# Optimization experiments

Measured on AMD Instinct MI355X. Metric: run time of the kernel, lower is better.

Reference implementation:

```python
import jax, jax.numpy as jnp
import numpy as np

EMBED, HEADS, WIN, UP = 180, 6, 16, 4
HDIM = EMBED // HEADS

def _win_part(x, ws):
    # x: [B, H, W, C] -> [B*(H//ws)*(W//ws), ws, ws, C]
    B, H, W, C = x.shape
    x = x.reshape(B, H // ws, ws, W // ws, ws, C).transpose(0, 1, 3, 2, 4, 5)
    return x.reshape(-1, ws, ws, C)

def _win_rev(w, ws, H, W):
    # inverse of _win_part
    C = w.shape[-1]
    B = w.shape[0] // ((H // ws) * (W // ws))
    x = w.reshape(B, H // ws, W // ws, ws, ws, C).transpose(0, 1, 3, 2, 4, 5)
    return x.reshape(B, H, W, C)

def _ln(x, g, b):
    mu = x.mean(-1, keepdims=True)
    v = ((x - mu) ** 2).mean(-1, keepdims=True)
    return (x - mu) * jax.lax.rsqrt(v + 1e-5) * g + b

def _forward(gumbel_u, x, sel1_w, sel1_b, sel2_w, sel2_b, sel3_w, sel3_b,
             embed_w, embed_b, ln1_g, ln1_b, qkv_w, qkv_b, proj_w, proj_b,
             ln2_g, ln2_b, mlp1_w, mlp1_b, mlp2_w, mlp2_b, up_w, up_b):
    B, C, H, W = x.shape
    ws = H // 4                                     # 64 -> 16 tiles per image
    tiles = _win_part(x.transpose(0, 2, 3, 1), ws)  # [T, ws, ws, C]
    T = tiles.shape[0]
    # --- TileSelection (pooled MLP router) ---
    pooled = tiles.reshape(T, 8, ws // 8, 8, ws // 8, C).mean((2, 4)).reshape(T, 8 * 8 * C)
    f1 = pooled @ sel1_w + sel1_b
    f2 = jax.nn.relu(f1) @ sel2_w + sel2_b
    f3 = jax.nn.relu(f2) @ sel3_w + sel3_b          # [T, 2] routing logits
    # --- hard gumbel-softmax with straight-through estimator (tau=1) ---
    g = -jnp.log(-jnp.log(gumbel_u + 1e-10) + 1e-10)
    y_soft = jax.nn.softmax(f3 + g, axis=-1)
    y_hard = jax.nn.one_hot(jnp.argmax(y_soft, -1), 2, dtype=y_soft.dtype)
    pi = jax.lax.stop_gradient(y_hard - y_soft) + y_soft
    mask = pi[:, 1]                                 # 1 -> transformer expert
    # --- TR expert (SwinIR-style block, dense dispatch over all tiles) ---
    tok = tiles.reshape(T, ws * ws, C) @ embed_w + embed_b   # [T, 4096, 180]
    h = _ln(tok, ln1_g, ln1_b)
    hw = _win_part(h.reshape(T, ws, ws, EMBED), WIN).reshape(-1, WIN * WIN, EMBED)
    Nw, L = hw.shape[0], WIN * WIN
    qkv = (hw @ qkv_w + qkv_b).reshape(Nw, L, 3, HEADS, HDIM)
    q, k, v = qkv[:, :, 0], qkv[:, :, 1], qkv[:, :, 2]
    attn = jax.nn.softmax(jnp.einsum('nlhd,nmhd->nhlm', q, k) / np.sqrt(HDIM).astype(np.float32), axis=-1)
    av = jnp.einsum('nhlm,nmhd->nlhd', attn, v).reshape(Nw, L, EMBED)
    av = av @ proj_w + proj_b
    av = _win_rev(av.reshape(Nw, WIN, WIN, EMBED), WIN, ws, ws).reshape(T, ws * ws, EMBED)
    tok = tok + av
    h2 = _ln(tok, ln2_g, ln2_b)
    tok = tok + jax.nn.gelu(h2 @ mlp1_w + mlp1_b) @ mlp2_w + mlp2_b
    # pixelshuffle x4 upsample: 180 -> 3*4*4
    up = (tok @ up_w + up_b).reshape(T, ws, ws, UP, UP, C)
    up = up.transpose(0, 1, 3, 2, 4, 5).reshape(T, ws * UP, ws * UP, C)
    # --- cheap expert: bicubic x4 ---
    neg = jax.image.resize(tiles, (T, ws * UP, ws * UP, C), method='bicubic')
    # --- combine per-tile and reassemble ---
    m = mask[:, None, None, None]
    sr_tiles = m * up + (1.0 - m) * neg             # [T, 4ws, 4ws, C]
    sr = _win_rev(sr_tiles, H, H * UP, W * UP)      # [B, 4H, 4W, C]
    return sr.transpose(0, 3, 1, 2), f3, f2, f1

def setup_inputs() -> dict:
    key = jax.random.key(0)
    ks = jax.random.split(key, 16)
    B, C, H, W = 1, 3, 256, 256
    T = B * 16
    p = lambda k, s: jax.random.normal(k, s, jnp.float32) * 0.02
    return {
        'x': jax.random.normal(ks[0], (B, C, H, W), jnp.float32),
        'gumbel_u': jax.random.uniform(ks[1], (T, 2), jnp.float32),
        'sel1_w': p(ks[2], (192, 64)), 'sel1_b': jnp.zeros((64,), jnp.float32),
        'sel2_w': p(ks[3], (64, 32)), 'sel2_b': jnp.zeros((32,), jnp.float32),
        'sel3_w': p(ks[4], (32, 2)), 'sel3_b': jnp.zeros((2,), jnp.float32),
        'embed_w': p(ks[5], (3, EMBED)), 'embed_b': jnp.zeros((EMBED,), jnp.float32),
        'ln1_g': jnp.ones((EMBED,), jnp.float32), 'ln1_b': jnp.zeros((EMBED,), jnp.float32),
        'qkv_w': p(ks[6], (EMBED, 3 * EMBED)), 'qkv_b': jnp.zeros((3 * EMBED,), jnp.float32),
        'proj_w': p(ks[7], (EMBED, EMBED)), 'proj_b': jnp.zeros((EMBED,), jnp.float32),
        'ln2_g': jnp.ones((EMBED,), jnp.float32), 'ln2_b': jnp.zeros((EMBED,), jnp.float32),
        'mlp1_w': p(ks[8], (EMBED, 2 * EMBED)), 'mlp1_b': jnp.zeros((2 * EMBED,), jnp.float32),
        'mlp2_w': p(ks[9], (2 * EMBED, EMBED)), 'mlp2_b': jnp.zeros((EMBED,), jnp.float32),
        'up_w': p(ks[10], (EMBED, 3 * UP * UP)), 'up_b': jnp.zeros((3 * UP * UP,), jnp.float32),
    }

def reference(x, gumbel_u, sel1_w, sel1_b, sel2_w, sel2_b, sel3_w, sel3_b,
              embed_w, embed_b, ln1_g, ln1_b, qkv_w, qkv_b, proj_w, proj_b,
              ln2_g, ln2_b, mlp1_w, mlp1_b, mlp2_w, mlp2_b, up_w, up_b):
    return _forward(gumbel_u, x, sel1_w, sel1_b, sel2_w, sel2_b, sel3_w, sel3_b,
                    embed_w, embed_b, ln1_g, ln1_b, qkv_w, qkv_b, proj_w, proj_b,
                    ln2_g, ln2_b, mlp1_w, mlp1_b, mlp2_w, mlp2_b, up_w, up_b)
```

## Files before the change

kernel.cpp:

```cpp
#include <hip/hip_runtime.h>
#include <hip/hip_bf16.h>
#include <cstdint>

typedef __hip_bfloat16 bf16;
typedef __attribute__((ext_vector_type(8))) short short8;
typedef __attribute__((ext_vector_type(4))) short short4v;
typedef __attribute__((ext_vector_type(4))) float f32x4;
typedef __attribute__((ext_vector_type(2))) unsigned int uint2v;

__device__ __forceinline__ float bf2f(bf16 v) { return __bfloat162float(v); }
__device__ __forceinline__ bf16  f2bf(float v) { return __float2bfloat16(v); }
__device__ __forceinline__ float rbf(short s) {
  union { uint32_t u; float f; } c; c.u = ((uint32_t)(uint16_t)s) << 16; return c.f;
}
__device__ __forceinline__ uint32_t pack2(float a, float b) {
  bf16 x = f2bf(a), y = f2bf(b);
  return (uint32_t)(*(uint16_t*)&x) | ((uint32_t)(*(uint16_t*)&y) << 16);
}
__device__ __forceinline__ uint2v pack4(float a, float b, float c, float d) {
  uint2v r; r[0] = pack2(a, b); r[1] = pack2(c, d); return r;
}
__device__ __forceinline__ int swz(int row, int g) { return g ^ (row & 7); }

__device__ __forceinline__ int win_to_token(int m) {
  int n = m >> 8, l = m & 255;
  int t = n >> 4, win = n & 15;
  int wi = win >> 2, wj = win & 3;
  int u = l >> 4, v = l & 15;
  return (t << 12) | ((wi * 16 + u) << 6) | (wj * 16 + v);
}

__global__ __launch_bounds__(256) void k_packsel(
    const float* __restrict__ qkvw, const float* __restrict__ projw,
    const float* __restrict__ mlp1w, const float* __restrict__ mlp2w,
    const float* __restrict__ upw, const float* __restrict__ qkvb,
    bf16* __restrict__ Bt_qkv, bf16* __restrict__ Bt_proj,
    bf16* __restrict__ Bt_mlp1, bf16* __restrict__ Bt_mlp2,
    bf16* __restrict__ Bt_up, float* __restrict__ biasq,
    const float* __restrict__ x, const float* __restrict__ gu,
    const float* __restrict__ s1w, const float* __restrict__ s1b,
    const float* __restrict__ s2w, const float* __restrict__ s2b,
    const float* __restrict__ s3w, const float* __restrict__ s3b,
    float* __restrict__ f1o, float* __restrict__ f2o, float* __restrict__ f3o,
    float* __restrict__ maskp) {
  if (blockIdx.x < 1203) {
    int idx = blockIdx.x * 256 + threadIdx.x;
    const int e0 = 576 * 192, e1 = e0 + 192 * 192, e2 = e1 + 384 * 192,
              e3 = e2 + 192 * 384, e4 = e3 + 64 * 192, e5 = e4 + 576;
    if (idx < e0) {
      int np = idx / 192, k = idx % 192;
      int buf = np / 192, colp = np % 192;
      int hd = colp >> 5, dd = colp & 31;
      float v = 0.f;
      if (dd < 30 && k < 180) v = qkvw[(size_t)k * 540 + buf * 180 + hd * 30 + dd];
      Bt_qkv[idx] = f2bf(v);
    } else if (idx < e1) {
      int off = idx - e0; int n = off / 192, kp = off % 192;
      int hd = kp >> 5, dd = kp & 31;
      float v = (dd < 30 && n < 180) ? projw[(size_t)(hd * 30 + dd) * 180 + n] : 0.f;
      Bt_proj[off] = f2bf(v);
    } else if (idx < e2) {
      int off = idx - e1; int n = off / 192, k = off % 192;
      Bt_mlp1[off] = f2bf((k < 180 && n < 360) ? mlp1w[(size_t)k * 360 + n] : 0.f);
    } else if (idx < e3) {
      int off = idx - e2; int n = off / 384, k = off % 384;
      Bt_mlp2[off] = f2bf((k < 360 && n < 180) ? mlp2w[(size_t)k * 180 + n] : 0.f);
    } else if (idx < e4) {
      int off = idx - e3; int n = off / 192, k = off % 192;
      Bt_up[off] = f2bf((k < 180 && n < 48) ? upw[(size_t)k * 48 + n] : 0.f);
    } else if (idx < e5) {
      int np = idx - e4;
      int buf = np / 192, colp = np % 192;
      int hd = colp >> 5, dd = colp & 31;
      biasq[np] = (dd < 30) ? qkvb[buf * 180 + hd * 30 + dd] : 0.f;
    }
    return;
  }
  int t = blockIdx.x - 1203;
  int tid = threadIdx.x;
  int th = t >> 2, tw = t & 3;
  __shared__ float pooled[192];
  __shared__ float red[256];
  __shared__ float f1s[64], f2s[32], f3s[2];
  if (tid < 192) {
    int ch = tid % 3, j = (tid / 3) & 7, i = tid / 24;
    const float* xp = x + ch * 65536 + (th * 64 + i * 8) * 256 + (tw * 64 + j * 8);
    float s = 0.f;
#pragma unroll
    for (int a = 0; a < 8; ++a)
#pragma unroll
      for (int b = 0; b < 8; ++b) s += xp[a * 256 + b];
    pooled[tid] = s * (1.0f / 64.0f);
  }
  __syncthreads();
  {
    int o = tid & 63, part = tid >> 6;
    float s = 0.f;
    for (int k = part * 48; k < part * 48 + 48; ++k) s = fmaf(pooled[k], s1w[k * 64 + o], s);
    red[tid] = s;
  }
  __syncthreads();
  if (tid < 64) {
    float v = red[tid] + red[tid + 64] + red[tid + 128] + red[tid + 192] + s1b[tid];
    f1o[t * 64 + tid] = v;
    f1s[tid] = fmaxf(v, 0.f);
  }
  __syncthreads();
  {
    int o = tid & 31, part = tid >> 5;
    float s = 0.f;
    for (int k = part * 8; k < part * 8 + 8; ++k) s = fmaf(f1s[k], s2w[k * 32 + o], s);
    red[tid] = s;
  }
  __syncthreads();
  if (tid < 32) {
    float v = s2b[tid];
#pragma unroll
    for (int p = 0; p < 8; ++p) v += red[tid + p * 32];
    f2o[t * 32 + tid] = v;
    f2s[tid] = fmaxf(v, 0.f);
  }
  __syncthreads();
  if (tid < 2) {
    float s = s3b[tid];
    for (int k = 0; k < 32; ++k) s = fmaf(f2s[k], s3w[k * 2 + tid], s);
    f3o[t * 2 + tid] = s;
    f3s[tid] = s;
  }
  __syncthreads();
  if (tid == 0) {
    float g0 = -logf(-logf(gu[t * 2 + 0] + 1e-10f) + 1e-10f);
    float g1 = -logf(-logf(gu[t * 2 + 1] + 1e-10f) + 1e-10f);
    maskp[t] = (f3s[1] + g1 > f3s[0] + g0) ? 1.0f : 0.0f;
  }
}

__global__ __launch_bounds__(256) void k_embed(
    const float* __restrict__ x, const float* __restrict__ ew,
    const float* __restrict__ eb, const float* __restrict__ g1,
    const float* __restrict__ b1, bf16* __restrict__ tok,
    bf16* __restrict__ Aq) {
  int wrow = blockIdx.x * 4 + (threadIdx.x >> 6);
  int lane = threadIdx.x & 63;
  int token = win_to_token(wrow);
  int t = token >> 12, p = token & 4095;
  int r = p >> 6, c = p & 63;
  int gh = (t >> 2) * 64 + r, gw = (t & 3) * 64 + c;
  float x0 = x[gh * 256 + gw];
  float x1 = x[65536 + gh * 256 + gw];
  float x2 = x[131072 + gh * 256 + gw];
  float v[3];
  float s = 0.f, s2 = 0.f;
#pragma unroll
  for (int i = 0; i < 3; ++i) {
    int e = lane + i * 64;
    float vv = 0.f;
    if (e < 180) {
      vv = eb[e];
      vv = fmaf(x0, ew[e], vv);
      vv = fmaf(x1, ew[180 + e], vv);
      vv = fmaf(x2, ew[360 + e], vv);
      tok[(size_t)wrow * 180 + e] = f2bf(vv);
      s += vv; s2 = fmaf(vv, vv, s2);
    }
    v[i] = vv;
  }
#pragma unroll
  for (int off = 32; off; off >>= 1) { s += __shfl_xor(s, off); s2 += __shfl_xor(s2, off); }
  float mu = s * (1.f / 180.f);
  float rs = rsqrtf(s2 * (1.f / 180.f) - mu * mu + 1e-5f);
#pragma unroll
  for (int i = 0; i < 3; ++i) {
    int e = lane + i * 64;
    if (e < 192) {
      float a = (e < 180) ? ((v[i] - mu) * rs * g1[e] + b1[e]) : 0.f;
      Aq[(size_t)wrow * 192 + e] = f2bf(a);
    }
  }
}

__global__ __launch_bounds__(256) void k_qkv2(
    const bf16* __restrict__ A, const bf16* __restrict__ Bt,
    const float* __restrict__ biasq, bf16* __restrict__ Qp,
    bf16* __restrict__ Kp, bf16* __restrict__ Vp) {
  __shared__ bf16 Bs[2][64 * 192];
  const int tid = threadIdx.x;
  const int w = tid >> 6, l = tid & 63;
  const int lr = l & 15, lk = l >> 4;
  const int rbase = blockIdx.x * 128 + w * 32 + lr;

  short8 fa[2][6];
#pragma unroll
  for (int i = 0; i < 2; ++i) {
    const bf16* Ab = A + (size_t)(rbase + i * 16) * 192 + lk * 8;
#pragma unroll
    for (int ks = 0; ks < 6; ++ks) fa[i][ks] = *(const short8*)(Ab + ks * 32);
  }

  {
    const bf16* src = Bt;
#pragma unroll
    for (int it = 0; it < 6; ++it) {
      int c = tid + it * 256;
      int n = c / 24, g = c % 24;
      *(short8*)&Bs[0][n * 192 + swz(n, g) * 8] = *(const short8*)(src + n * 192 + g * 8);
    }
  }

  for (int nt = 0; nt < 9; ++nt) {
    __syncthreads();
    if (nt < 8) {
      const bf16* src = Bt + (size_t)(nt + 1) * 64 * 192;
      bf16* dstb = Bs[(nt + 1) & 1];
#pragma unroll
      for (int it = 0; it < 6; ++it) {
        int c = tid + it * 256;
        int n = c / 24, g = c % 24;
        *(short8*)&dstb[n * 192 + swz(n, g) * 8] = *(const short8*)(src + n * 192 + g * 8);
      }
    }
    const bf16* Bb = Bs[nt & 1];
    f32x4 acc[2][4];
#pragma unroll
    for (int i = 0; i < 2; ++i)
#pragma unroll
      for (int j = 0; j < 4; ++j) acc[i][j] = (f32x4){0.f, 0.f, 0.f, 0.f};
#pragma unroll
    for (int ks = 0; ks < 6; ++ks) {
      short8 fb[4];
#pragma unroll
      for (int j = 0; j < 4; ++j) {
        int rn = j * 16 + lr;
        fb[j] = *(const short8*)&Bb[rn * 192 + swz(rn, ks * 4 + lk) * 8];
      }
#pragma unroll
      for (int i = 0; i < 2; ++i)
#pragma unroll
        for (int j = 0; j < 4; ++j)
          acc[i][j] = __builtin_amdgcn_mfma_f32_16x16x32_bf16(fb[j], fa[i][ks], acc[i][j], 0, 0, 0);
    }
    bf16* dst = (nt < 3) ? Qp : (nt < 6) ? Kp : Vp;
    int c0 = (nt % 3) * 64;
#pragma unroll
    for (int i = 0; i < 2; ++i) {
      int row = rbase + i * 16;
#pragma unroll
      for (int j = 0; j < 4; ++j) {
        int np = nt * 64 + j * 16 + lk * 4;
        f32x4 bv = *(const f32x4*)&biasq[np];
        *(uint2v*)(dst + (size_t)row * 192 + c0 + j * 16 + lk * 4) =
            pack4(acc[i][j][0] + bv[0], acc[i][j][1] + bv[1],
                  acc[i][j][2] + bv[2], acc[i][j][3] + bv[3]);
      }
    }
  }
}

__global__ __launch_bounds__(256) void k_attn2(
    const bf16* __restrict__ Qp, const bf16* __restrict__ Kp,
    const bf16* __restrict__ Vp, bf16* __restrict__ av) {
  const int blk = blockIdx.x;
  const int win = blk / 6, hd = blk % 6;
  const int tid = threadIdx.x;
  const int w = tid >> 6, l = tid & 63;
  const int lr = l & 15, lk = l >> 4;
  const float scale = 0.18257418583505536f;

  __shared__ bf16 Ks[256][40];
  __shared__ bf16 Vs[32][264];
  __shared__ bf16 Ps[4][16][264];

  {
    const bf16* src = Kp + (size_t)(win * 256 + tid) * 192 + hd * 32;
#pragma unroll
    for (int c = 0; c < 4; ++c)
      *(short8*)&Ks[tid][c * 8] = *(const short8*)(src + c * 8);
  }
  {
    const bf16* src = Vp + (size_t)(win * 256 + tid) * 192 + hd * 32;
    short8 vv[4];
#pragma unroll
    for (int c = 0; c < 4; ++c) vv[c] = *(const short8*)(src + c * 8);
#pragma unroll
    for (int c = 0; c < 4; ++c)
#pragma unroll
      for (int e = 0; e < 8; ++e)
        *(short*)&Vs[c * 8 + e][tid] = vv[c][e];
  }
  __syncthreads();

  for (int qt = 0; qt < 4; ++qt) {
    const int qbase = qt * 64 + w * 16;
    short8 fq = *(const short8*)(Qp + (size_t)(win * 256 + qbase + lr) * 192 + hd * 32 + lk * 8);
    f32x4 accS[16];
#pragma unroll
    for (int kt = 0; kt < 16; ++kt) {
      short8 fk = *(const short8*)(&Ks[kt * 16 + lr][lk * 8]);
      accS[kt] = __builtin_amdgcn_mfma_f32_16x16x32_bf16(
          fk, fq, (f32x4){0.f, 0.f, 0.f, 0.f}, 0, 0, 0);
    }
    float mraw = -1e30f;
#pragma unroll
    for (int kt = 0; kt < 16; ++kt)
#pragma unroll
      for (int r = 0; r < 4; ++r) mraw = fmaxf(mraw, accS[kt][r]);
    mraw = fmaxf(mraw, __shfl_xor(mraw, 16));
    mraw = fmaxf(mraw, __shfl_xor(mraw, 32));
    const float mc = mraw * scale;
    float lsum = 0.f;
#pragma unroll
    for (int kt = 0; kt < 16; ++kt) {
      float p0 = __expf(fmaf(accS[kt][0], scale, -mc));
      float p1 = __expf(fmaf(accS[kt][1], scale, -mc));
      float p2 = __expf(fmaf(accS[kt][2], scale, -mc));
      float p3 = __expf(fmaf(accS[kt][3], scale, -mc));
      lsum += (p0 + p1) + (p2 + p3);
      *(uint32_t*)&Ps[w][lr][kt * 16 + lk * 4]     = pack2(p0, p1);
      *(uint32_t*)&Ps[w][lr][kt * 16 + lk * 4 + 2] = pack2(p2, p3);
    }
    lsum += __shfl_xor(lsum, 16);
    lsum += __shfl_xor(lsum, 32);
    __syncthreads();
    f32x4 accO0 = (f32x4){0.f, 0.f, 0.f, 0.f};
    f32x4 accO1 = (f32x4){0.f, 0.f, 0.f, 0.f};
#pragma unroll
    for (int ks = 0; ks < 8; ++ks) {
      short8 fp  = *(const short8*)(&Ps[w][lr][ks * 32 + lk * 8]);
      short8 fv0 = *(const short8*)(&Vs[lr][ks * 32 + lk * 8]);
      short8 fv1 = *(const short8*)(&Vs[16 + lr][ks * 32 + lk * 8]);
      accO0 = __builtin_amdgcn_mfma_f32_16x16x32_bf16(fv0, fp, accO0, 0, 0, 0);
      accO1 = __builtin_amdgcn_mfma_f32_16x16x32_bf16(fv1, fp, accO1, 0, 0, 0);
    }
    float invl = 1.f / lsum;
    bf16* avrow = av + (size_t)(win * 256 + qbase + lr) * 192 + hd * 32;
    *(uint2v*)(avrow + lk * 4) =
        pack4(accO0[0] * invl, accO0[1] * invl, accO0[2] * invl, accO0[3] * invl);
    *(uint2v*)(avrow + 16 + lk * 4) =
        pack4(accO1[0] * invl, accO1[1] * invl, accO1[2] * invl, accO1[3] * invl);
    __syncthreads();
  }
}

__global__ __launch_bounds__(256) void k_post(
    const bf16* __restrict__ av, const bf16* __restrict__ tok,
    const bf16* __restrict__ Btp, const float* __restrict__ pb,
    const float* __restrict__ g2, const float* __restrict__ b2,
    const bf16* __restrict__ Bt1, const float* __restrict__ b1m,
    const bf16* __restrict__ Bt2, const float* __restrict__ b2m,
    const bf16* __restrict__ Btu, const float* __restrict__ bu,
    bf16* __restrict__ up) {
  __shared__ bf16 Bs[64 * 192];
  __shared__ bf16 T2[64 * 192];
  __shared__ bf16 Hm[64 * 192];
  const int tid = threadIdx.x;
  const int w = tid >> 6, l = tid & 63;
  const int lr = l & 15, lk = l >> 4;
  const int row_l = w * 16 + lr;
  const int row_g = blockIdx.x * 64 + row_l;
  const int half = (lk & 1) * 4;

  short8 fa[6];
  {
    const bf16* ab = av + (size_t)row_g * 192 + lk * 8;
#pragma unroll
    for (int ks = 0; ks < 6; ++ks) fa[ks] = *(const short8*)(ab + ks * 32);
  }

  f32x4 t2v[3][4];
#pragma unroll
  for (int nt = 0; nt < 3; ++nt) {
    __syncthreads();
    for (int c = tid; c < 1536; c += 256) {
      int n = c / 24, g = c % 24;
      *(short8*)&Bs[n * 192 + swz(n, g) * 8] =
          *(const short8*)(Btp + (size_t)(nt * 64 + n) * 192 + g * 8);
    }
    __syncthreads();
    f32x4 acc[4];
#pragma unroll
    for (int j = 0; j < 4; ++j) acc[j] = (f32x4){0.f, 0.f, 0.f, 0.f};
#pragma unroll
    for (int ks = 0; ks < 6; ++ks) {
      short8 fb[4];
#pragma unroll
      for (int j = 0; j < 4; ++j) {
        int rn = j * 16 + lr;
        fb[j] = *(const short8*)&Bs[rn * 192 + swz(rn, ks * 4 + lk) * 8];
      }
#pragma unroll
      for (int j = 0; j < 4; ++j)
        acc[j] = __builtin_amdgcn_mfma_f32_16x16x32_bf16(fb[j], fa[ks], acc[j], 0, 0, 0);
    }
#pragma unroll
    for (int j = 0; j < 4; ++j) {
      int n = nt * 64 + j * 16 + lk * 4;
      if (n < 180) {
        f32x4 bv = *(const f32x4*)&pb[n];
        short4v tv = *(const short4v*)(tok + (size_t)row_g * 180 + n);
#pragma unroll
        for (int q = 0; q < 4; ++q) t2v[nt][j][q] = acc[j][q] + bv[q] + rbf(tv[q]);
      } else {
        t2v[nt][j] = (f32x4){0.f, 0.f, 0.f, 0.f};
      }
    }
  }

  {
    float s = 0.f, s2 = 0.f;
#pragma unroll
    for (int nt = 0; nt < 3; ++nt)
#pragma unroll
      for (int j = 0; j < 4; ++j)
#pragma unroll
        for (int q = 0; q < 4; ++q) { float v = t2v[nt][j][q]; s += v; s2 = fmaf(v, v, s2); }
    s += __shfl_xor(s, 16);  s += __shfl_xor(s, 32);
    s2 += __shfl_xor(s2, 16); s2 += __shfl_xor(s2, 32);
    float mu = s * (1.f / 180.f);
    float rs = rsqrtf(s2 * (1.f / 180.f) - mu * mu + 1e-5f);
#pragma unroll
    for (int nt = 0; nt < 3; ++nt)
#pragma unroll
      for (int j = 0; j < 4; ++j) {
        int n = nt * 64 + j * 16 + lk * 4;
        float h[4] = {0.f, 0.f, 0.f, 0.f};
        if (n < 180) {
          f32x4 gv = *(const f32x4*)&g2[n];
          f32x4 bv = *(const f32x4*)&b2[n];
#pragma unroll
          for (int q = 0; q < 4; ++q) h[q] = (t2v[nt][j][q] - mu) * rs * gv[q] + bv[q];
        }
        int g = nt * 8 + j * 2 + (lk >> 1);
        *(uint2v*)&Hm[row_l * 192 + swz(row_l, g) * 8 + half] = pack4(h[0], h[1], h[2], h[3]);
      }
  }
  __syncthreads();
  short8 fh[6];
#pragma unroll
  for (int ks = 0; ks < 6; ++ks)
    fh[ks] = *(const short8*)&Hm[row_l * 192 + swz(row_l, ks * 4 + lk) * 8];

  f32x4 acc2[3][4];
#pragma unroll
  for (int t = 0; t < 3; ++t)
#pragma unroll
    for (int j = 0; j < 4; ++j) acc2[t][j] = (f32x4){0.f, 0.f, 0.f, 0.f};
#pragma unroll
  for (int nt = 0; nt < 6; ++nt) {
    __syncthreads();
    for (int c = tid; c < 1536; c += 256) {
      int n = c / 24, g = c % 24;
      *(short8*)&Bs[n * 192 + swz(n, g) * 8] =
          *(const short8*)(Bt1 + (size_t)(nt * 64 + n) * 192 + g * 8);
    }
    __syncthreads();
    f32x4 acc1[4];
#pragma unroll
    for (int j = 0; j < 4; ++j) acc1[j] = (f32x4){0.f, 0.f, 0.f, 0.f};
#pragma unroll
    for (int ks = 0; ks < 6; ++ks) {
      short8 fb[4];
#pragma unroll
      for (int j = 0; j < 4; ++j) {
        int rn = j * 16 + lr;
        fb[j] = *(const short8*)&Bs[rn * 192 + swz(rn, ks * 4 + lk) * 8];
      }
#pragma unroll
      for (int j = 0; j < 4; ++j)
        acc1[j] = __builtin_amdgcn_mfma_f32_16x16x32_bf16(fb[j], fh[ks], acc1[j], 0, 0, 0);
    }
#pragma unroll
    for (int j = 0; j < 4; ++j) {
      int n = nt * 64 + j * 16 + lk * 4;
      float m4[4] = {0.f, 0.f, 0.f, 0.f};
      if (n < 360) {
        f32x4 bv = *(const f32x4*)&b1m[n];
#pragma unroll
        for (int q = 0; q < 4; ++q) {
          float v = acc1[j][q] + bv[q];
          float u = 0.7978845608028654f * (v + 0.044715f * v * v * v);
          m4[q] = v / (1.f + __expf(-2.f * u));
        }
      }
      int g = j * 2 + (lk >> 1);
      *(uint2v*)&Hm[row_l * 192 + swz(row_l, g) * 8 + half] = pack4(m4[0], m4[1], m4[2], m4[3]);
    }
    __syncthreads();
    for (int c = tid; c < 1536; c += 256) {
      int n = c / 8, g = c % 8;
      *(short8*)&Bs[n * 64 + swz(n, g) * 8] =
          *(const short8*)(Bt2 + (size_t)n * 384 + nt * 64 + g * 8);
    }
    __syncthreads();
    short8 fm[2];
#pragma unroll
    for (int s = 0; s < 2; ++s)
      fm[s] = *(const short8*)&Hm[row_l * 192 + swz(row_l, s * 4 + lk) * 8];
#pragma unroll
    for (int s = 0; s < 2; ++s)
#pragma unroll
      for (int t = 0; t < 3; ++t)
#pragma unroll
        for (int j = 0; j < 4; ++j) {
          int rn = t * 64 + j * 16 + lr;
          short8 fb2 = *(const short8*)&Bs[rn * 64 + swz(rn, s * 4 + lk) * 8];
          acc2[t][j] = __builtin_amdgcn_mfma_f32_16x16x32_bf16(fb2, fm[s], acc2[t][j], 0, 0, 0);
        }
  }

#pragma unroll
  for (int t = 0; t < 3; ++t)
#pragma unroll
    for (int j = 0; j < 4; ++j) {
      int n = t * 64 + j * 16 + lk * 4;
      float o4[4] = {0.f, 0.f, 0.f, 0.f};
      if (n < 180) {
        f32x4 bv = *(const f32x4*)&b2m[n];
#pragma unroll
        for (int q = 0; q < 4; ++q) o4[q] = acc2[t][j][q] + bv[q] + t2v[t][j][q];
      }
      int g = t * 8 + j * 2 + (lk >> 1);
      *(uint2v*)&T2[row_l * 192 + swz(row_l, g) * 8 + half] = pack4(o4[0], o4[1], o4[2], o4[3]);
    }
  __syncthreads();

  for (int c = tid; c < 1536; c += 256) {
    int n = c / 24, g = c % 24;
    *(short8*)&Bs[n * 192 + swz(n, g) * 8] =
        *(const short8*)(Btu + (size_t)n * 192 + g * 8);
  }
  __syncthreads();
  short8 ft[6];
#pragma unroll
  for (int ks = 0; ks < 6; ++ks)
    ft[ks] = *(const short8*)&T2[row_l * 192 + swz(row_l, ks * 4 + lk) * 8];
  f32x4 acc3[3];
#pragma unroll
  for (int j = 0; j < 3; ++j) acc3[j] = (f32x4){0.f, 0.f, 0.f, 0.f};
#pragma unroll
  for (int ks = 0; ks < 6; ++ks) {
    short8 fb[3];
#pragma unroll
    for (int j = 0; j < 3; ++j) {
      int rn = j * 16 + lr;
      fb[j] = *(const short8*)&Bs[rn * 192 + swz(rn, ks * 4 + lk) * 8];
    }
#pragma unroll
    for (int j = 0; j < 3; ++j)
      acc3[j] = __builtin_amdgcn_mfma_f32_16x16x32_bf16(fb[j], ft[ks], acc3[j], 0, 0, 0);
  }
#pragma unroll
  for (int j = 0; j < 3; ++j) {
    int n = j * 16 + lk * 4;
    f32x4 bv = *(const f32x4*)&bu[n];
    *(uint2v*)(up + (size_t)row_g * 48 + n) =
        pack4(acc3[j][0] + bv[0], acc3[j][1] + bv[1], acc3[j][2] + bv[2], acc3[j][3] + bv[3]);
  }
}

__device__ const float c_cubw[4][4] = {
    {-0.0439453125f, 0.3896484375f, 0.7275390625f, -0.0732421875f},
    {-0.0068359375f, 0.0908203125f, 0.9638671875f, -0.0478515625f},
    {-0.0478515625f, 0.9638671875f, 0.0908203125f, -0.0068359375f},
    {-0.0732421875f, 0.7275390625f, 0.3896484375f, -0.0439453125f},
};

__device__ __forceinline__ void cubw(int r, int ph, float* w, int& base) {
  base = r + ((ph < 2) ? -2 : -1);
  float sum = 0.f;
#pragma unroll
  for (int i = 0; i < 4; ++i) {
    int idx = base + i;
    float wi = (idx >= 0 && idx < 64) ? c_cubw[ph][i] : 0.f;
    w[i] = wi; sum += wi;
  }
  float inv = 1.f / sum;
#pragma unroll
  for (int i = 0; i < 4; ++i) w[i] *= inv;
}

__global__ __launch_bounds__(256) void k_blend(
    const bf16* __restrict__ up, const float* __restrict__ x,
    const float* __restrict__ maskp, float* __restrict__ sr) {
  int idx = blockIdx.x * 256 + threadIdx.x;
  int ch = idx >> 20;
  int rem = idx & 1048575;
  int gR = rem >> 10, gC = rem & 1023;
  int th = gR >> 8, tw = gC >> 8;
  int t = th * 4 + tw;
  int R = gR & 255, C = gC & 255;
  int r = R >> 2, a = R & 3, c = C >> 2, b = C & 3;
  float m = maskp[t];
  float outv;
  if (m > 0.5f) {
    int wi = r >> 4, u = r & 15, wj = c >> 4, v = c & 15;
    int wrow = (t * 16 + wi * 4 + wj) * 256 + u * 16 + v;
    outv = bf2f(up[(size_t)wrow * 48 + a * 12 + b * 3 + ch]);
  } else {
    float wy[4], wx[4];
    int yb, xb;
    cubw(r, a, wy, yb);
    cubw(c, b, wx, xb);
    const float* xc = x + ch * 65536;
    float neg = 0.f;
#pragma unroll
    for (int i = 0; i < 4; ++i) {
      int yi = yb + i;
      if (yi < 0 || yi > 63) continue;
      float rowsum = 0.f;
#pragma unroll
      for (int j = 0; j < 4; ++j) {
        int xj = xb + j;
        if (xj < 0 || xj > 63) continue;
        rowsum = fmaf(wx[j], xc[(th * 64 + yi) * 256 + tw * 64 + xj], rowsum);
      }
      neg = fmaf(wy[i], rowsum, neg);
    }
    outv = neg;
  }
  sr[idx] = outv;
}

extern "C" void kernel_launch(void* const* d_in, const int* in_sizes, int n_in,
                              void* d_out, int out_size, void* d_ws, size_t ws_size,
                              hipStream_t stream) {
  const float* x     = (const float*)d_in[0];
  const float* gu    = (const float*)d_in[1];
  const float* s1w   = (const float*)d_in[2];
  const float* s1b   = (const float*)d_in[3];
  const float* s2w   = (const float*)d_in[4];
  const float* s2b   = (const float*)d_in[5];
  const float* s3w   = (const float*)d_in[6];
  const float* s3b   = (const float*)d_in[7];
  const float* ew    = (const float*)d_in[8];
  const float* ebias = (const float*)d_in[9];
  const float* ln1g  = (const float*)d_in[10];
  const float* ln1b  = (const float*)d_in[11];
  const float* qkvw  = (const float*)d_in[12];
  const float* qkvb  = (const float*)d_in[13];
  const float* projw = (const float*)d_in[14];
  const float* projb = (const float*)d_in[15];
  const float* ln2g  = (const float*)d_in[16];
  const float* ln2b  = (const float*)d_in[17];
  const float* mlp1w = (const float*)d_in[18];
  const float* mlp1b = (const float*)d_in[19];
  const float* mlp2w = (const float*)d_in[20];
  const float* mlp2b = (const float*)d_in[21];
  const float* upw   = (const float*)d_in[22];
  const float* upb   = (const float*)d_in[23];

  float* out = (float*)d_out;
  float* sr  = out;
  float* f3o = out + 3145728;
  float* f2o = f3o + 32;
  float* f1o = f2o + 512;

  char* ws = (char*)d_ws;
  bf16* tok  = (bf16*)(ws);
  bf16* ABuf = (bf16*)(ws + 23592960);
  bf16* Qp   = (bf16*)(ws + 48758784);
  bf16* Kp   = (bf16*)(ws + 73924608);
  bf16* Vp   = (bf16*)(ws + 99090432);
  float* maskp   = (float*)(ws + 124256256);
  bf16* Bt_qkv  = (bf16*)(ws + 124256320);
  bf16* Bt_proj = (bf16*)(ws + 124477504);
  bf16* Bt_mlp1 = (bf16*)(ws + 124551232);
  bf16* Bt_mlp2 = (bf16*)(ws + 124698688);
  bf16* Bt_up   = (bf16*)(ws + 124846144);
  float* biasq  = (float*)(ws + 124870720);
  bf16* up      = (bf16*)(ws + 124873088);
  bf16* av = ABuf;

  k_packsel<<<1219, 256, 0, stream>>>(qkvw, projw, mlp1w, mlp2w, upw, qkvb,
                                      Bt_qkv, Bt_proj, Bt_mlp1, Bt_mlp2, Bt_up, biasq,
                                      x, gu, s1w, s1b, s2w, s2b, s3w, s3b,
                                      f1o, f2o, f3o, maskp);
  k_embed<<<16384, 256, 0, stream>>>(x, ew, ebias, ln1g, ln1b, tok, ABuf);
  k_qkv2<<<512, 256, 0, stream>>>(ABuf, Bt_qkv, biasq, Qp, Kp, Vp);
  k_attn2<<<1536, 256, 0, stream>>>(Qp, Kp, Vp, av);
  k_post<<<1024, 256, 0, stream>>>(av, tok, Bt_proj, projb, ln2g, ln2b,
                                   Bt_mlp1, mlp1b, Bt_mlp2, mlp2b, Bt_up, upb, up);
  k_blend<<<12288, 256, 0, stream>>>(up, x, maskp, sr);
}
```

Measured before the change: 226.8 us.

## Shuffle softmax probabilities in registers and alias LDS buffers in post kernel

The attention kernel no longer stages the probability matrix through shared memory. It rebuilds the MFMA operand layout with cross-lane shuffles, which also removes two block-wide barriers per query tile. The post kernel reuses the Hm buffer in place of a separate T2 buffer and adds one barrier before the reuse. Both changes cut LDS footprint, which can allow more resident blocks, at the cost of many extra shuffle instructions and higher register pressure from the 32 packed values held per lane.

```diff
diff --git a/kernel.cpp b/kernel.cpp
--- a/kernel.cpp
+++ b/kernel.cpp
@@ -7,6 +7,7 @@
 typedef __attribute__((ext_vector_type(4))) short short4v;
 typedef __attribute__((ext_vector_type(4))) float f32x4;
 typedef __attribute__((ext_vector_type(2))) unsigned int uint2v;
+typedef __attribute__((ext_vector_type(4))) unsigned int uint4v;
 
 __device__ __forceinline__ float bf2f(bf16 v) { return __bfloat162float(v); }
 __device__ __forceinline__ bf16  f2bf(float v) { return __float2bfloat16(v); }
@@ -256,7 +257,7 @@
   }
 }
 
-__global__ __launch_bounds__(256) void k_attn2(
+__global__ __launch_bounds__(256) void k_attn3(
     const bf16* __restrict__ Qp, const bf16* __restrict__ Kp,
     const bf16* __restrict__ Vp, bf16* __restrict__ av) {
   const int blk = blockIdx.x;
@@ -268,7 +269,6 @@
 
   __shared__ bf16 Ks[256][40];
   __shared__ bf16 Vs[32][264];
-  __shared__ bf16 Ps[4][16][264];
 
   {
     const bf16* src = Kp + (size_t)(win * 256 + tid) * 192 + hd * 32;
@@ -288,6 +288,10 @@
         *(short*)&Vs[c * 8 + e][tid] = vv[c][e];
   }
   __syncthreads();
+
+  const int a0lane = lr + 32 * (lk & 1);
+  const int a1lane = a0lane + 16;
+  const bool hi = (lk >= 2);
 
   for (int qt = 0; qt < 4; ++qt) {
     const int qbase = qt * 64 + w * 16;
@@ -308,6 +312,7 @@
     mraw = fmaxf(mraw, __shfl_xor(mraw, 32));
     const float mc = mraw * scale;
     float lsum = 0.f;
+    uint32_t u0[16], u1[16];
 #pragma unroll
     for (int kt = 0; kt < 16; ++kt) {
       float p0 = __expf(fmaf(accS[kt][0], scale, -mc));
@@ -315,17 +320,30 @@
       float p2 = __expf(fmaf(accS[kt][2], scale, -mc));
       float p3 = __expf(fmaf(accS[kt][3], scale, -mc));
       lsum += (p0 + p1) + (p2 + p3);
-      *(uint32_t*)&Ps[w][lr][kt * 16 + lk * 4]     = pack2(p0, p1);
-      *(uint32_t*)&Ps[w][lr][kt * 16 + lk * 4 + 2] = pack2(p2, p3);
+      u0[kt] = pack2(p0, p1);
+      u1[kt] = pack2(p2, p3);
     }
     lsum += __shfl_xor(lsum, 16);
     lsum += __shfl_xor(lsum, 32);
-    __syncthreads();
     f32x4 accO0 = (f32x4){0.f, 0.f, 0.f, 0.f};
     f32x4 accO1 = (f32x4){0.f, 0.f, 0.f, 0.f};
 #pragma unroll
     for (int ks = 0; ks < 8; ++ks) {
-      short8 fp  = *(const short8*)(&Ps[w][lr][ks * 32 + lk * 8]);
+      uint32_t A0 = (uint32_t)__shfl((int)u0[2 * ks], a0lane);
+      uint32_t A1 = (uint32_t)__shfl((int)u1[2 * ks], a0lane);
+      uint32_t A2 = (uint32_t)__shfl((int)u0[2 * ks], a1lane);
+      uint32_t A3 = (uint32_t)__shfl((int)u1[2 * ks], a1lane);
+      uint32_t B0 = (uint32_t)__shfl((int)u0[2 * ks + 1], a0lane);
+      uint32_t B1 = (uint32_t)__shfl((int)u1[2 * ks + 1], a0lane);
+      uint32_t B2 = (uint32_t)__shfl((int)u0[2 * ks + 1], a1lane);
+      uint32_t B3 = (uint32_t)__shfl((int)u1[2 * ks + 1], a1lane);
+      uint4v Dv;
+      Dv[0] = hi ? B0 : A0;
+      Dv[1] = hi ? B1 : A1;
+      Dv[2] = hi ? B2 : A2;
+      Dv[3] = hi ? B3 : A3;
+      short8 fp;
+      __builtin_memcpy(&fp, &Dv, 16);
       short8 fv0 = *(const short8*)(&Vs[lr][ks * 32 + lk * 8]);
       short8 fv1 = *(const short8*)(&Vs[16 + lr][ks * 32 + lk * 8]);
       accO0 = __builtin_amdgcn_mfma_f32_16x16x32_bf16(fv0, fp, accO0, 0, 0, 0);
@@ -337,7 +355,6 @@
         pack4(accO0[0] * invl, accO0[1] * invl, accO0[2] * invl, accO0[3] * invl);
     *(uint2v*)(avrow + 16 + lk * 4) =
         pack4(accO1[0] * invl, accO1[1] * invl, accO1[2] * invl, accO1[3] * invl);
-    __syncthreads();
   }
 }
 
@@ -350,7 +367,6 @@
     const bf16* __restrict__ Btu, const float* __restrict__ bu,
     bf16* __restrict__ up) {
   __shared__ bf16 Bs[64 * 192];
-  __shared__ bf16 T2[64 * 192];
   __shared__ bf16 Hm[64 * 192];
   const int tid = threadIdx.x;
   const int w = tid >> 6, l = tid & 63;
@@ -507,6 +523,7 @@
         }
   }
 
+  __syncthreads();
 #pragma unroll
   for (int t = 0; t < 3; ++t)
 #pragma unroll
@@ -519,7 +536,7 @@
         for (int q = 0; q < 4; ++q) o4[q] = acc2[t][j][q] + bv[q] + t2v[t][j][q];
       }
       int g = t * 8 + j * 2 + (lk >> 1);
-      *(uint2v*)&T2[row_l * 192 + swz(row_l, g) * 8 + half] = pack4(o4[0], o4[1], o4[2], o4[3]);
+      *(uint2v*)&Hm[row_l * 192 + swz(row_l, g) * 8 + half] = pack4(o4[0], o4[1], o4[2], o4[3]);
     }
   __syncthreads();
 
@@ -532,7 +549,7 @@
   short8 ft[6];
 #pragma unroll
   for (int ks = 0; ks < 6; ++ks)
-    ft[ks] = *(const short8*)&T2[row_l * 192 + swz(row_l, ks * 4 + lk) * 8];
+    ft[ks] = *(const short8*)&Hm[row_l * 192 + swz(row_l, ks * 4 + lk) * 8];
   f32x4 acc3[3];
 #pragma unroll
   for (int j = 0; j < 3; ++j) acc3[j] = (f32x4){0.f, 0.f, 0.f, 0.f};
@@ -676,7 +693,7 @@
                                       f1o, f2o, f3o, maskp);
   k_embed<<<16384, 256, 0, stream>>>(x, ew, ebias, ln1g, ln1b, tok, ABuf);
   k_qkv2<<<512, 256, 0, stream>>>(ABuf, Bt_qkv, biasq, Qp, Kp, Vp);
-  k_attn2<<<1536, 256, 0, stream>>>(Qp, Kp, Vp, av);
+  k_attn3<<<1536, 256, 0, stream>>>(Qp, Kp, Vp, av);
   k_post<<<1024, 256, 0, stream>>>(av, tok, Bt_proj, projb, ln2g, ln2b,
                                    Bt_mlp1, mlp1b, Bt_mlp2, mlp2b, Bt_up, upb, up);
   k_blend<<<12288, 256, 0, stream>>>(up, x, maskp, sr);
```

Result: slower. 245.6 us (+8.3%).

## Double-buffer weight staging in k_post to overlap loads with MFMA

Applied to the files above, without the earlier changes.

Splits the shared weight buffer in k_post into two halves, so the next weight tile (proj, mlp1, mlp2 slice, upsample) is copied into one half while MFMAs read the other. This removes one barrier per step and lets global loads overlap compute. The separate T2 buffer is dropped and Hm is reused, which keeps shared memory the same. The cost is a more intricate barrier ordering, which risks races if any buffer is reused too early.

```diff
diff --git a/kernel.cpp b/kernel.cpp
--- a/kernel.cpp
+++ b/kernel.cpp
@@ -349,8 +349,7 @@
     const bf16* __restrict__ Bt2, const float* __restrict__ b2m,
     const bf16* __restrict__ Btu, const float* __restrict__ bu,
     bf16* __restrict__ up) {
-  __shared__ bf16 Bs[64 * 192];
-  __shared__ bf16 T2[64 * 192];
+  __shared__ bf16 Bs[2][64 * 192];
   __shared__ bf16 Hm[64 * 192];
   const int tid = threadIdx.x;
   const int w = tid >> 6, l = tid & 63;
@@ -359,6 +358,30 @@
   const int row_g = blockIdx.x * 64 + row_l;
   const int half = (lk & 1) * 4;
 
+#define STAGE_A(srcp, dstb)                                               \
+  {                                                                       \
+    const bf16* _s = (srcp);                                              \
+    bf16* _d = (dstb);                                                    \
+    _Pragma("unroll")                                                     \
+    for (int it = 0; it < 6; ++it) {                                      \
+      int c = tid + it * 256;                                             \
+      int n = c / 24, g = c % 24;                                         \
+      *(short8*)&_d[n * 192 + swz(n, g) * 8] =                            \
+          *(const short8*)(_s + (size_t)n * 192 + g * 8);                 \
+    }                                                                     \
+  }
+#define STAGE_S(ntv, dstb)                                                \
+  {                                                                       \
+    bf16* _d = (dstb);                                                    \
+    _Pragma("unroll")                                                     \
+    for (int it = 0; it < 6; ++it) {                                      \
+      int c = tid + it * 256;                                             \
+      int n = c / 8, g = c % 8;                                           \
+      *(short8*)&_d[n * 64 + swz(n, g) * 8] =                             \
+          *(const short8*)(Bt2 + (size_t)n * 384 + (ntv) * 64 + g * 8);   \
+    }                                                                     \
+  }
+
   short8 fa[6];
   {
     const bf16* ab = av + (size_t)row_g * 192 + lk * 8;
@@ -367,15 +390,15 @@
   }
 
   f32x4 t2v[3][4];
+
+  STAGE_A(Btp, Bs[0]);
+
 #pragma unroll
   for (int nt = 0; nt < 3; ++nt) {
     __syncthreads();
-    for (int c = tid; c < 1536; c += 256) {
-      int n = c / 24, g = c % 24;
-      *(short8*)&Bs[n * 192 + swz(n, g) * 8] =
-          *(const short8*)(Btp + (size_t)(nt * 64 + n) * 192 + g * 8);
-    }
-    __syncthreads();
+    if (nt < 2) { STAGE_A(Btp + (size_t)(nt + 1) * 64 * 192, Bs[(nt + 1) & 1]); }
+    else        { STAGE_A(Bt1, Bs[1]); }
+    const bf16* Bb = Bs[nt & 1];
     f32x4 acc[4];
 #pragma unroll
     for (int j = 0; j < 4; ++j) acc[j] = (f32x4){0.f, 0.f, 0.f, 0.f};
@@ -385,7 +408,7 @@
 #pragma unroll
       for (int j = 0; j < 4; ++j) {
         int rn = j * 16 + lr;
-        fb[j] = *(const short8*)&Bs[rn * 192 + swz(rn, ks * 4 + lk) * 8];
+        fb[j] = *(const short8*)&Bb[rn * 192 + swz(rn, ks * 4 + lk) * 8];
       }
 #pragma unroll
       for (int j = 0; j < 4; ++j)
@@ -433,80 +456,79 @@
         *(uint2v*)&Hm[row_l * 192 + swz(row_l, g) * 8 + half] = pack4(h[0], h[1], h[2], h[3]);
       }
   }
-  __syncthreads();
+
   short8 fh[6];
-#pragma unroll
-  for (int ks = 0; ks < 6; ++ks)
-    fh[ks] = *(const short8*)&Hm[row_l * 192 + swz(row_l, ks * 4 + lk) * 8];
-
   f32x4 acc2[3][4];
 #pragma unroll
   for (int t = 0; t < 3; ++t)
 #pragma unroll
     for (int j = 0; j < 4; ++j) acc2[t][j] = (f32x4){0.f, 0.f, 0.f, 0.f};
+
 #pragma unroll
   for (int nt = 0; nt < 6; ++nt) {
     __syncthreads();
-    for (int c = tid; c < 1536; c += 256) {
-      int n = c / 24, g = c % 24;
-      *(short8*)&Bs[n * 192 + swz(n, g) * 8] =
-          *(const short8*)(Bt1 + (size_t)(nt * 64 + n) * 192 + g * 8);
+    STAGE_S(nt, Bs[0]);
+    if (nt == 0) {
+#pragma unroll
+      for (int ks = 0; ks < 6; ++ks)
+        fh[ks] = *(const short8*)&Hm[row_l * 192 + swz(row_l, ks * 4 + lk) * 8];
+    }
+    {
+      const bf16* Bb = Bs[1];
+      f32x4 acc1[4];
+#pragma unroll
+      for (int j = 0; j < 4; ++j) acc1[j] = (f32x4){0.f, 0.f, 0.f, 0.f};
+#pragma unroll
+      for (int ks = 0; ks < 6; ++ks) {
+        short8 fb[4];
+#pragma unroll
+        for (int j = 0; j < 4; ++j) {
+          int rn = j * 16 + lr;
+          fb[j] = *(const short8*)&Bb[rn * 192 + swz(rn, ks * 4 + lk) * 8];
+        }
+#pragma unroll
+        for (int j = 0; j < 4; ++j)
+          acc1[j] = __builtin_amdgcn_mfma_f32_16x16x32_bf16(fb[j], fh[ks], acc1[j], 0, 0, 0);
+      }
+#pragma unroll
+      for (int j = 0; j < 4; ++j) {
+        int n = nt * 64 + j * 16 + lk * 4;
+        float m4[4] = {0.f, 0.f, 0.f, 0.f};
+        if (n < 360) {
+          f32x4 bv = *(const f32x4*)&b1m[n];
+#pragma unroll
+          for (int q = 0; q < 4; ++q) {
+            float v = acc1[j][q] + bv[q];
+            float u = 0.7978845608028654f * (v + 0.044715f * v * v * v);
+            m4[q] = v / (1.f + __expf(-2.f * u));
+          }
+        }
+        int g = j * 2 + (lk >> 1);
+        *(uint2v*)&Hm[row_l * 192 + swz(row_l, g) * 8 + half] = pack4(m4[0], m4[1], m4[2], m4[3]);
+      }
     }
     __syncthreads();
-    f32x4 acc1[4];
-#pragma unroll
-    for (int j = 0; j < 4; ++j) acc1[j] = (f32x4){0.f, 0.f, 0.f, 0.f};
-#pragma unroll
-    for (int ks = 0; ks < 6; ++ks) {
-      short8 fb[4];
-#pragma unroll
-      for (int j = 0; j < 4; ++j) {
-        int rn = j * 16 + lr;
-        fb[j] = *(const short8*)&Bs[rn * 192 + swz(rn, ks * 4 + lk) * 8];
-      }
-#pragma unroll
-      for (int j = 0; j < 4; ++j)
-        acc1[j] = __builtin_amdgcn_mfma_f32_16x16x32_bf16(fb[j], fh[ks], acc1[j], 0, 0, 0);
-    }
-#pragma unroll
-    for (int j = 0; j < 4; ++j) {
-      int n = nt * 64 + j * 16 + lk * 4;
-      float m4[4] = {0.f, 0.f, 0.f, 0.f};
-      if (n < 360) {
-        f32x4 bv = *(const f32x4*)&b1m[n];
-#pragma unroll
-        for (int q = 0; q < 4; ++q) {
-          float v = acc1[j][q] + bv[q];
-          float u = 0.7978845608028654f * (v + 0.044715f * v * v * v);
-          m4[q] = v / (1.f + __expf(-2.f * u));
-        }
-      }
-      int g = j * 2 + (lk >> 1);
-      *(uint2v*)&Hm[row_l * 192 + swz(row_l, g) * 8 + half] = pack4(m4[0], m4[1], m4[2], m4[3]);
-    }
-    __syncthreads();
-    for (int c = tid; c < 1536; c += 256) {
-      int n = c / 8, g = c % 8;
-      *(short8*)&Bs[n * 64 + swz(n, g) * 8] =
-          *(const short8*)(Bt2 + (size_t)n * 384 + nt * 64 + g * 8);
-    }
-    __syncthreads();
-    short8 fm[2];
-#pragma unroll
-    for (int s = 0; s < 2; ++s)
-      fm[s] = *(const short8*)&Hm[row_l * 192 + swz(row_l, s * 4 + lk) * 8];
-#pragma unroll
-    for (int s = 0; s < 2; ++s)
-#pragma unroll
-      for (int t = 0; t < 3; ++t)
-#pragma unroll
-        for (int j = 0; j < 4; ++j) {
-          int rn = t * 64 + j * 16 + lr;
-          short8 fb2 = *(const short8*)&Bs[rn * 64 + swz(rn, s * 4 + lk) * 8];
-          acc2[t][j] = __builtin_amdgcn_mfma_f32_16x16x32_bf16(fb2, fm[s], acc2[t][j], 0, 0, 0);
-        }
-  }
-
+    if (nt < 5) { STAGE_A(Bt1 + (size_t)(nt + 1) * 64 * 192, Bs[1]); }
+    else        { STAGE_A(Btu, Bs[1]); }
+    {
+      short8 fm[2];
+#pragma unroll
+      for (int s = 0; s < 2; ++s)
+        fm[s] = *(const short8*)&Hm[row_l * 192 + swz(row_l, s * 4 + lk) * 8];
+#pragma unroll
+      for (int s = 0; s < 2; ++s)
+#pragma unroll
+        for (int t = 0; t < 3; ++t)
+#pragma unroll
+          for (int j = 0; j < 4; ++j) {
+            int rn = t * 64 + j * 16 + lr;
+            short8 fb2 = *(const short8*)&Bs[0][rn * 64 + swz(rn, s * 4 + lk) * 8];
+            acc2[t][j] = __builtin_amdgcn_mfma_f32_16x16x32_bf16(fb2, fm[s], acc2[t][j], 0, 0, 0);
+          }
+    }
+  }
+
+  __syncthreads();
 #pragma unroll
   for (int t = 0; t < 3; ++t)
 #pragma unroll
@@ -519,20 +541,14 @@
         for (int q = 0; q < 4; ++q) o4[q] = acc2[t][j][q] + bv[q] + t2v[t][j][q];
       }
       int g = t * 8 + j * 2 + (lk >> 1);
-      *(uint2v*)&T2[row_l * 192 + swz(row_l, g) * 8 + half] = pack4(o4[0], o4[1], o4[2], o4[3]);
-    }
-  __syncthreads();
-
-  for (int c = tid; c < 1536; c += 256) {
-    int n = c / 24, g = c % 24;
-    *(short8*)&Bs[n * 192 + swz(n, g) * 8] =
-        *(const short8*)(Btu + (size_t)n * 192 + g * 8);
-  }
-  __syncthreads();
+      *(uint2v*)&Hm[row_l * 192 + swz(row_l, g) * 8 + half] = pack4(o4[0], o4[1], o4[2], o4[3]);
+    }
+  __syncthreads();
+
   short8 ft[6];
 #pragma unroll
   for (int ks = 0; ks < 6; ++ks)
-    ft[ks] = *(const short8*)&T2[row_l * 192 + swz(row_l, ks * 4 + lk) * 8];
+    ft[ks] = *(const short8*)&Hm[row_l * 192 + swz(row_l, ks * 4 + lk) * 8];
   f32x4 acc3[3];
 #pragma unroll
   for (int j = 0; j < 3; ++j) acc3[j] = (f32x4){0.f, 0.f, 0.f, 0.f};
@@ -542,7 +558,7 @@
 #pragma unroll
     for (int j = 0; j < 3; ++j) {
       int rn = j * 16 + lr;
-      fb[j] = *(const short8*)&Bs[rn * 192 + swz(rn, ks * 4 + lk) * 8];
+      fb[j] = *(const short8*)&Bs[1][rn * 192 + swz(rn, ks * 4 + lk) * 8];
     }
 #pragma unroll
     for (int j = 0; j < 3; ++j)
@@ -555,6 +571,8 @@
     *(uint2v*)(up + (size_t)row_g * 48 + n) =
         pack4(acc3[j][0] + bv[0], acc3[j][1] + bv[1], acc3[j][2] + bv[2], acc3[j][3] + bv[3]);
   }
+#undef STAGE_A
+#undef STAGE_S
 }
 
 __device__ const float c_cubw[4][4] = {
```

New measurement: 215.0 us. 5.2% less time.
